# Performance work log

Hardware: AMD Instinct MI355X
Metric: run time of the kernel (lower is better)

Reference implementation:

```python
import jax, jax.numpy as jnp
import numpy as np

E, D, DFF = 8, 1024, 4096

def setup_inputs() -> dict:
    key = jax.random.key(0)
    ks = jax.random.split(key, 10)
    s = 0.02
    return {
        "x":  jax.random.normal(ks[0], (4, 2048, D), dtype=jnp.float32),
        "Wr": jax.random.normal(ks[1], (D, E), dtype=jnp.float32) * s,
        "br": jnp.zeros((E,), dtype=jnp.float32),
        "W1": jax.random.normal(ks[2], (E, D, DFF), dtype=jnp.float32) * s,
        "b1": jnp.zeros((E, DFF), dtype=jnp.float32),
        "W2": jax.random.normal(ks[3], (E, D, DFF), dtype=jnp.float32) * s,
        "b2": jnp.zeros((E, DFF), dtype=jnp.float32),
        "W3": jax.random.normal(ks[4], (E, DFF, D), dtype=jnp.float32) * s,
        "b3": jnp.zeros((E, D), dtype=jnp.float32),
    }

def reference(x, Wr, br, W1, b1, W2, b2, W3, b3):
    b, s, d = x.shape
    xt = x.reshape(b * s, d)                       # [T, D]
    logits = xt @ Wr + br                          # [T, E]
    pr, idx = jax.lax.top_k(logits, 2)             # [T, 2]
    w = jax.nn.softmax(pr, axis=-1)                # softmax over the 2 selected experts
    # combine weight per (token, expert): sum of routing weights where expert selected
    onehot = jax.nn.one_hot(idx, W1.shape[0], dtype=x.dtype)  # [T, 2, E]
    cw = jnp.einsum('tk,tke->te', w, onehot)       # [T, E]
    y = jnp.zeros_like(xt)
    for e in range(W1.shape[0]):                   # small fixed expert loop
        h = jax.nn.silu(xt @ W1[e] + b1[e]) * (xt @ W2[e] + b2[e])  # SwiGLU [T, DFF]
        y = y + (h @ W3[e] + b3[e]) * cw[:, e:e + 1]
    return y.reshape(b, s, d)
```

## Files before the change

kernel.cpp:

```cpp
#include <hip/hip_runtime.h>

#define T_TOK 8192
#define DIM   1024
#define DFF_  4096
#define NE    8
#define MAXT  144

typedef float  f32x4 __attribute__((ext_vector_type(4)));
typedef __bf16 b16x8 __attribute__((ext_vector_type(8)));
typedef unsigned short u16x4 __attribute__((ext_vector_type(4)));

__device__ __forceinline__ unsigned short f2bf(float f) {
  union { float f; unsigned int u; } v; v.f = f;
  unsigned int r = v.u + 0x7fffu + ((v.u >> 16) & 1u);
  return (unsigned short)(r >> 16);
}

__device__ __forceinline__ void gload_lds16(const void* g, void* l) {
  __builtin_amdgcn_global_load_lds((const __attribute__((address_space(1))) void*)g,
                                   (__attribute__((address_space(3))) void*)l,
                                   16, 0, 0);
}

#define DRAIN_VMCNT() asm volatile("s_waitcnt vmcnt(0)" ::: "memory")

__global__ __launch_bounds__(256) void transpose_cvt(const float* __restrict__ src,
                                                     unsigned short* __restrict__ dst,
                                                     int R, int C) {
  __shared__ float tile[64][68];
  size_t mat = (size_t)blockIdx.z * R * C;
  int c0 = blockIdx.x * 64, r0 = blockIdx.y * 64;
  int t = threadIdx.x;
  int rcol = (t & 15) * 4, rrow = t >> 4;
  const float* s = src + mat + (size_t)r0 * C + c0;
#pragma unroll
  for (int i = 0; i < 4; i++) {
    int r = rrow + i * 16;
    f32x4 v = *(const f32x4*)(s + (size_t)r * C + rcol);
    *(f32x4*)(&tile[r][rcol]) = v;
  }
  __syncthreads();
  unsigned short* d = dst + mat + (size_t)c0 * R + r0;
  int wrow4 = (t & 15) * 4, wcol = t >> 4;
#pragma unroll
  for (int i = 0; i < 4; i++) {
    int cc = wcol + i * 16;
    u16x4 o;
    o[0] = f2bf(tile[wrow4 + 0][cc]);
    o[1] = f2bf(tile[wrow4 + 1][cc]);
    o[2] = f2bf(tile[wrow4 + 2][cc]);
    o[3] = f2bf(tile[wrow4 + 3][cc]);
    *(u16x4*)(&d[(size_t)cc * R + wrow4]) = o;
  }
}

__global__ __launch_bounds__(256) void router_k(const float* __restrict__ x,
                                                const float* __restrict__ Wr,
                                                const float* __restrict__ br,
                                                unsigned short* __restrict__ Xbf,
                                                int* __restrict__ top2e,
                                                float* __restrict__ top2w,
                                                int* __restrict__ counts) {
  __shared__ int lcnt[NE];
  if (threadIdx.x < NE) lcnt[threadIdx.x] = 0;
  __syncthreads();
  int wid = threadIdx.x >> 6, lane = threadIdx.x & 63;
  int t = blockIdx.x * 4 + wid;
  const float* xr = x + (size_t)t * DIM;
  unsigned short* xb = Xbf + (size_t)t * DIM;
  float s[NE];
#pragma unroll
  for (int e = 0; e < NE; e++) s[e] = 0.f;
  for (int i = 0; i < DIM / 64; i++) {
    int dd = i * 64 + lane;
    float xv = xr[dd];
    xb[dd] = f2bf(xv);
    const float* w = Wr + (size_t)dd * NE;
#pragma unroll
    for (int e = 0; e < NE; e++) s[e] += xv * w[e];
  }
#pragma unroll
  for (int m = 32; m >= 1; m >>= 1) {
#pragma unroll
    for (int e = 0; e < NE; e++) s[e] += __shfl_xor(s[e], m, 64);
  }
  if (lane == 0) {
#pragma unroll
    for (int e = 0; e < NE; e++) s[e] += br[e];
    int e0 = 0;
#pragma unroll
    for (int e = 1; e < NE; e++) if (s[e] > s[e0]) e0 = e;
    int e1 = (e0 == 0) ? 1 : 0;
#pragma unroll
    for (int e = 0; e < NE; e++) if (e != e0 && s[e] > s[e1]) e1 = e;
    float w0 = 1.f / (1.f + expf(s[e1] - s[e0]));
    top2e[2 * t] = e0; top2e[2 * t + 1] = e1;
    top2w[2 * t] = w0; top2w[2 * t + 1] = 1.f - w0;
    atomicAdd(&lcnt[e0], 1);
    atomicAdd(&lcnt[e1], 1);
  }
  __syncthreads();
  if (threadIdx.x < NE) atomicAdd(&counts[threadIdx.x], lcnt[threadIdx.x]);
}

__global__ void scan_build(int* __restrict__ ctrl) {
  if (threadIdx.x != 0 || blockIdx.x != 0) return;
  int* counts = ctrl;
  int* offsets = ctrl + 8;
  int* cursors = ctrl + 16;
  int* nt256 = ctrl + 24;
  int* nt128 = ctrl + 25;
  int* tE256 = ctrl + 32;
  int* tM256 = ctrl + 32 + MAXT;
  int* tE128 = ctrl + 32 + 2 * MAXT;
  int* tM128 = ctrl + 32 + 3 * MAXT;
  int o = 0;
  for (int e = 0; e < NE; e++) { offsets[e] = o; cursors[e] = o; o += counts[e]; }
  int a = 0, b = 0;
  for (int e = 0; e < NE; e++) {
    for (int m0 = 0; m0 < counts[e]; m0 += 256) { tE256[a] = e; tM256[a] = m0; a++; }
    for (int m0 = 0; m0 < counts[e]; m0 += 128) { tE128[b] = e; tM128[b] = m0; b++; }
  }
  nt256[0] = a;
  nt128[0] = b;
}

__global__ __launch_bounds__(256) void scatter_k(const int* __restrict__ top2e,
                                                 const float* __restrict__ top2w,
                                                 int* __restrict__ cursors,
                                                 int* __restrict__ list_tok,
                                                 float* __restrict__ list_w) {
  __shared__ int lcnt[NE];
  __shared__ int lbase[NE];
  int tid = threadIdx.x;
  if (tid < NE) lcnt[tid] = 0;
  __syncthreads();
  int t = blockIdx.x * 256 + tid;
  int e0 = top2e[2 * t], e1 = top2e[2 * t + 1];
  int r0 = atomicAdd(&lcnt[e0], 1);
  int r1 = atomicAdd(&lcnt[e1], 1);
  __syncthreads();
  if (tid < NE) lbase[tid] = atomicAdd(&cursors[tid], lcnt[tid]);
  __syncthreads();
  int p0 = lbase[e0] + r0, p1 = lbase[e1] + r1;
  list_tok[p0] = t; list_w[p0] = top2w[2 * t];
  list_tok[p1] = t; list_w[p1] = top2w[2 * t + 1];
}

__global__ __launch_bounds__(1024, 4) void gemm1_k(const unsigned short* __restrict__ Xbf,
                                                   const unsigned short* __restrict__ W1T,
                                                   const unsigned short* __restrict__ W2T,
                                                   const float* __restrict__ b1,
                                                   const float* __restrict__ b2,
                                                   unsigned short* __restrict__ H,
                                                   const int* __restrict__ list_tok,
                                                   const int* __restrict__ ctrl) {
  const int* counts = ctrl; const int* offsets = ctrl + 8;
  const int* ntile = ctrl + 24;
  const int* tileE = ctrl + 32; const int* tileM = ctrl + 32 + MAXT;
  int bt = blockIdx.y;
  if (bt >= ntile[0]) return;
  int e = tileE[bt], m0 = tileM[bt];
  int Me = counts[e], off = offsets[e];
  int n0 = blockIdx.x * 128;

  __shared__ unsigned short lds[2][32768];

  int tid = threadIdx.x, lane = tid & 63, wid = tid >> 6;
  int wr = wid >> 2, wc = wid & 3;

  const unsigned short* gsrc[4];
  unsigned ldsoff[4];
  {
    int lr = lane >> 3;
    int sc = ((lane & 7) ^ (lane >> 3)) * 8;
#pragma unroll
    for (int j = 0; j < 4; j++) {
      int c = wid * 4 + j;
      ldsoff[j] = c * 512;
      if (c < 32) {
        int r = c * 8 + lr;
        int tok = (m0 + r < Me) ? list_tok[off + m0 + r] : list_tok[off];
        gsrc[j] = Xbf + (size_t)tok * DIM + sc;
      } else if (c < 48) {
        int n = n0 + (c - 32) * 8 + lr;
        gsrc[j] = W1T + ((size_t)e * DFF_ + n) * DIM + sc;
      } else {
        int n = n0 + (c - 48) * 8 + lr;
        gsrc[j] = W2T + ((size_t)e * DFF_ + n) * DIM + sc;
      }
    }
  }

  unsigned aoff[2][4], boff[2][2];
  {
    int colg = lane >> 4;
#pragma unroll
    for (int kk = 0; kk < 2; kk++) {
#pragma unroll
      for (int m = 0; m < 4; m++) {
        int row = wr * 64 + m * 16 + (lane & 15);
        aoff[kk][m] = row * 64 + (((kk * 4 + colg) ^ (row & 7)) * 8);
      }
#pragma unroll
      for (int n = 0; n < 2; n++) {
        int row = wc * 32 + n * 16 + (lane & 15);
        boff[kk][n] = 16384 + row * 64 + (((kk * 4 + colg) ^ (row & 7)) * 8);
      }
    }
  }

  f32x4 acc1[4][2], acc2[4][2];
#pragma unroll
  for (int i = 0; i < 4; i++)
#pragma unroll
    for (int j = 0; j < 2; j++) {
      acc1[i][j] = f32x4{0.f, 0.f, 0.f, 0.f};
      acc2[i][j] = f32x4{0.f, 0.f, 0.f, 0.f};
    }

  auto compute = [&](const unsigned short* base) {
#pragma unroll
    for (int kk = 0; kk < 2; kk++) {
      b16x8 aF[4], bF1[2], bF2[2];
#pragma unroll
      for (int m = 0; m < 4; m++) aF[m] = *(const b16x8*)(base + aoff[kk][m]);
#pragma unroll
      for (int n = 0; n < 2; n++) {
        bF1[n] = *(const b16x8*)(base + boff[kk][n]);
        bF2[n] = *(const b16x8*)(base + boff[kk][n] + 8192);
      }
#pragma unroll
      for (int m = 0; m < 4; m++)
#pragma unroll
        for (int n = 0; n < 2; n++) {
          acc1[m][n] = __builtin_amdgcn_mfma_f32_16x16x32_bf16(aF[m], bF1[n], acc1[m][n], 0, 0, 0);
          acc2[m][n] = __builtin_amdgcn_mfma_f32_16x16x32_bf16(aF[m], bF2[n], acc2[m][n], 0, 0, 0);
        }
    }
  };

#pragma unroll
  for (int j = 0; j < 4; j++) gload_lds16(gsrc[j], (void*)(&lds[0][ldsoff[j]]));
  DRAIN_VMCNT();
  __syncthreads();

  int cur = 0;
  const int NK = DIM / 64;
  for (int kt = 0; kt < NK; kt++) {
    if (kt + 1 < NK) {
#pragma unroll
      for (int j = 0; j < 4; j++)
        gload_lds16(gsrc[j] + (kt + 1) * 64, (void*)(&lds[cur ^ 1][ldsoff[j]]));
    }
    compute(&lds[cur][0]);
    DRAIN_VMCNT();
    __syncthreads();
    cur ^= 1;
  }

#pragma unroll
  for (int n = 0; n < 2; n++) {
    int col = n0 + wc * 32 + n * 16 + (lane & 15);
    float bb1 = b1[e * DFF_ + col], bb2 = b2[e * DFF_ + col];
#pragma unroll
    for (int m = 0; m < 4; m++) {
      int rbase = wr * 64 + m * 16 + (lane >> 4) * 4;
#pragma unroll
      for (int r = 0; r < 4; r++) {
        int rr = rbase + r;
        if (m0 + rr < Me) {
          float c1 = acc1[m][n][r] + bb1;
          float c2 = acc2[m][n][r] + bb2;
          float h = c1 * c2 / (1.f + __expf(-c1));
          H[(size_t)(off + m0 + rr) * DFF_ + col] = f2bf(h);
        }
      }
    }
  }
}

__global__ __launch_bounds__(512) void gemm2_k(const unsigned short* __restrict__ H,
                                               const unsigned short* __restrict__ W3T,
                                               const float* __restrict__ b3,
                                               const int* __restrict__ list_tok,
                                               const float* __restrict__ list_w,
                                               float* __restrict__ y,
                                               const int* __restrict__ ctrl) {
  const int* counts = ctrl; const int* offsets = ctrl + 8;
  const int* ntile = ctrl + 25;
  const int* tileE = ctrl + 32 + 2 * MAXT;
  const int* tileM = ctrl + 32 + 3 * MAXT;
  int bt = blockIdx.y;
  if (bt >= ntile[0]) return;
  int e = tileE[bt], m0 = tileM[bt];
  int Me = counts[e], off = offsets[e];
  int n0 = blockIdx.x * 128;

  __shared__ unsigned short lds[2][2 * 128 * 64];

  int tid = threadIdx.x, lane = tid & 63, wid = tid >> 6;
  int wr = wid >> 2, wc = wid & 3;

  const unsigned short* gsrc[4];
  unsigned ldsoff[4];
  {
    int lr = lane >> 3;
    int sc = ((lane & 7) ^ (lane >> 3)) * 8;
#pragma unroll
    for (int j = 0; j < 4; j++) {
      int c = wid * 4 + j;
      ldsoff[j] = c * 512;
      if (c < 16) {
        int r = c * 8 + lr;
        int pos = (m0 + r < Me) ? (off + m0 + r) : off;
        gsrc[j] = H + (size_t)pos * DFF_ + sc;
      } else {
        int n = n0 + (c - 16) * 8 + lr;
        gsrc[j] = W3T + ((size_t)e * DIM + n) * DFF_ + sc;
      }
    }
  }

  unsigned aoff[2][4], boff[2][2];
  {
    int colg = lane >> 4;
#pragma unroll
    for (int kk = 0; kk < 2; kk++) {
#pragma unroll
      for (int fi = 0; fi < 4; fi++) {
        int row = wr * 64 + fi * 16 + (lane & 15);
        aoff[kk][fi] = row * 64 + (((kk * 4 + colg) ^ (row & 7)) * 8);
      }
#pragma unroll
      for (int fj = 0; fj < 2; fj++) {
        int row = wc * 32 + fj * 16 + (lane & 15);
        boff[kk][fj] = 128 * 64 + row * 64 + (((kk * 4 + colg) ^ (row & 7)) * 8);
      }
    }
  }

  f32x4 acc[4][2];
#pragma unroll
  for (int i = 0; i < 4; i++)
#pragma unroll
    for (int j = 0; j < 2; j++) acc[i][j] = f32x4{0.f, 0.f, 0.f, 0.f};

  auto compute = [&](const unsigned short* base) {
#pragma unroll
    for (int kk = 0; kk < 2; kk++) {
      b16x8 aF[4], bF[2];
#pragma unroll
      for (int fi = 0; fi < 4; fi++) aF[fi] = *(const b16x8*)(base + aoff[kk][fi]);
#pragma unroll
      for (int fj = 0; fj < 2; fj++) bF[fj] = *(const b16x8*)(base + boff[kk][fj]);
#pragma unroll
      for (int fi = 0; fi < 4; fi++)
#pragma unroll
        for (int fj = 0; fj < 2; fj++)
          acc[fi][fj] = __builtin_amdgcn_mfma_f32_16x16x32_bf16(aF[fi], bF[fj], acc[fi][fj], 0, 0, 0);
    }
  };

#pragma unroll
  for (int j = 0; j < 4; j++) gload_lds16(gsrc[j], (void*)(&lds[0][ldsoff[j]]));
  DRAIN_VMCNT();
  __syncthreads();

  int cur = 0;
  const int NK = DFF_ / 64;
  for (int kt = 0; kt < NK; kt++) {
    if (kt + 1 < NK) {
#pragma unroll
      for (int j = 0; j < 4; j++)
        gload_lds16(gsrc[j] + (kt + 1) * 64, (void*)(&lds[cur ^ 1][ldsoff[j]]));
    }
    compute(&lds[cur][0]);
    DRAIN_VMCNT();
    __syncthreads();
    cur ^= 1;
  }

#pragma unroll
  for (int fi = 0; fi < 4; fi++)
#pragma unroll
    for (int fj = 0; fj < 2; fj++) {
      int col = n0 + wc * 32 + fj * 16 + (lane & 15);
      float bb3 = b3[e * DIM + col];
      int rbase = wr * 64 + fi * 16 + (lane >> 4) * 4;
#pragma unroll
      for (int r = 0; r < 4; r++) {
        int rr = rbase + r;
        if (m0 + rr < Me) {
          int pos = off + m0 + rr;
          float v = list_w[pos] * (acc[fi][fj][r] + bb3);
          atomicAdd(&y[(size_t)list_tok[pos] * DIM + col], v);
        }
      }
    }
}

extern "C" void kernel_launch(void* const* d_in, const int* in_sizes, int n_in,
                              void* d_out, int out_size, void* d_ws, size_t ws_size,
                              hipStream_t stream) {
  (void)in_sizes; (void)n_in; (void)ws_size;
  const float* x  = (const float*)d_in[0];
  const float* Wr = (const float*)d_in[1];
  const float* br = (const float*)d_in[2];
  const float* W1 = (const float*)d_in[3];
  const float* b1 = (const float*)d_in[4];
  const float* W2 = (const float*)d_in[5];
  const float* b2 = (const float*)d_in[6];
  const float* W3 = (const float*)d_in[7];
  const float* b3 = (const float*)d_in[8];
  float* y = (float*)d_out;
  char* ws = (char*)d_ws;

  const size_t matB = (size_t)NE * DFF_ * DIM * 2;
  size_t oW1T = 0;
  size_t oW2T = oW1T + matB;
  size_t oXbf = oW2T + matB;
  size_t oH   = oXbf + (size_t)T_TOK * DIM * 2;
  size_t oT2e = oH + (size_t)2 * T_TOK * DFF_ * 2;
  size_t oT2w = oT2e + (size_t)2 * T_TOK * 4;
  size_t oLtk = oT2w + (size_t)2 * T_TOK * 4;
  size_t oLw  = oLtk + (size_t)2 * T_TOK * 4;
  size_t oCtl = oLw + (size_t)2 * T_TOK * 4;

  unsigned short* W1T = (unsigned short*)(ws + oW1T);
  unsigned short* W2T = (unsigned short*)(ws + oW2T);
  unsigned short* W3T = (unsigned short*)(ws + oW1T);
  unsigned short* Xbf = (unsigned short*)(ws + oXbf);
  unsigned short* Hb  = (unsigned short*)(ws + oH);
  int*   top2e = (int*)(ws + oT2e);
  float* top2w = (float*)(ws + oT2w);
  int*   ltok  = (int*)(ws + oLtk);
  float* lw    = (float*)(ws + oLw);
  int*   ctrl  = (int*)(ws + oCtl);

  hipMemsetAsync(y, 0, (size_t)out_size * 4, stream);
  hipMemsetAsync(ctrl, 0, (32 + 4 * MAXT) * 4, stream);

  transpose_cvt<<<dim3(DFF_ / 64, DIM / 64, NE), 256, 0, stream>>>(W1, W1T, DIM, DFF_);
  transpose_cvt<<<dim3(DFF_ / 64, DIM / 64, NE), 256, 0, stream>>>(W2, W2T, DIM, DFF_);
  router_k<<<dim3(T_TOK / 4), 256, 0, stream>>>(x, Wr, br, Xbf, top2e, top2w, ctrl);
  scan_build<<<dim3(1), 64, 0, stream>>>(ctrl);
  scatter_k<<<dim3(T_TOK / 256), 256, 0, stream>>>(top2e, top2w, ctrl + 16, ltok, lw);
  gemm1_k<<<dim3(DFF_ / 128, 71), 1024, 0, stream>>>(Xbf, W1T, W2T, b1, b2, Hb, ltok, ctrl);
  transpose_cvt<<<dim3(DIM / 64, DFF_ / 64, NE), 256, 0, stream>>>(W3, W3T, DFF_, DIM);
  gemm2_k<<<dim3(DIM / 128, MAXT - 8), 512, 0, stream>>>(Hb, W3T, b3, ltok, lw, y, ctrl);
}
```

Before: 739.6 us.

## Enlarge gemm2 tiles to 256x256 with 1024 threads and shared 256-row tile list

The second expert GEMM moves from 128-row by 128-col tiles with 512 threads to 256-row by 256-col tiles with 1024 threads, reusing the 256-row tile list already built for gemm1. The 128-row tile list is dropped from the scan kernel and the control memset shrinks to match. Each wave now computes a 64x64 output block with 16 MFMA accumulators, which raises arithmetic intensity per LDS load and cuts the number of times H and W3T are reread. The cost is 128 KB of LDS per block and fewer blocks in flight, which lowers occupancy and increases padding waste for partially filled expert tiles.

```diff
diff --git a/kernel.cpp b/kernel.cpp
--- a/kernel.cpp
+++ b/kernel.cpp
@@ -109,20 +109,14 @@
   int* offsets = ctrl + 8;
   int* cursors = ctrl + 16;
   int* nt256 = ctrl + 24;
-  int* nt128 = ctrl + 25;
   int* tE256 = ctrl + 32;
   int* tM256 = ctrl + 32 + MAXT;
-  int* tE128 = ctrl + 32 + 2 * MAXT;
-  int* tM128 = ctrl + 32 + 3 * MAXT;
   int o = 0;
   for (int e = 0; e < NE; e++) { offsets[e] = o; cursors[e] = o; o += counts[e]; }
-  int a = 0, b = 0;
-  for (int e = 0; e < NE; e++) {
+  int a = 0;
+  for (int e = 0; e < NE; e++)
     for (int m0 = 0; m0 < counts[e]; m0 += 256) { tE256[a] = e; tM256[a] = m0; a++; }
-    for (int m0 = 0; m0 < counts[e]; m0 += 128) { tE128[b] = e; tM128[b] = m0; b++; }
-  }
   nt256[0] = a;
-  nt128[0] = b;
 }
 
 __global__ __launch_bounds__(256) void scatter_k(const int* __restrict__ top2e,
@@ -280,24 +274,23 @@
   }
 }
 
-__global__ __launch_bounds__(512) void gemm2_k(const unsigned short* __restrict__ H,
-                                               const unsigned short* __restrict__ W3T,
-                                               const float* __restrict__ b3,
-                                               const int* __restrict__ list_tok,
-                                               const float* __restrict__ list_w,
-                                               float* __restrict__ y,
-                                               const int* __restrict__ ctrl) {
+__global__ __launch_bounds__(1024, 4) void gemm2_k(const unsigned short* __restrict__ H,
+                                                   const unsigned short* __restrict__ W3T,
+                                                   const float* __restrict__ b3,
+                                                   const int* __restrict__ list_tok,
+                                                   const float* __restrict__ list_w,
+                                                   float* __restrict__ y,
+                                                   const int* __restrict__ ctrl) {
   const int* counts = ctrl; const int* offsets = ctrl + 8;
-  const int* ntile = ctrl + 25;
-  const int* tileE = ctrl + 32 + 2 * MAXT;
-  const int* tileM = ctrl + 32 + 3 * MAXT;
+  const int* ntile = ctrl + 24;
+  const int* tileE = ctrl + 32; const int* tileM = ctrl + 32 + MAXT;
   int bt = blockIdx.y;
   if (bt >= ntile[0]) return;
   int e = tileE[bt], m0 = tileM[bt];
   int Me = counts[e], off = offsets[e];
-  int n0 = blockIdx.x * 128;
-
-  __shared__ unsigned short lds[2][2 * 128 * 64];
+  int n0 = blockIdx.x * 256;
+
+  __shared__ unsigned short lds[2][32768];
 
   int tid = threadIdx.x, lane = tid & 63, wid = tid >> 6;
   int wr = wid >> 2, wc = wid & 3;
@@ -311,54 +304,54 @@
     for (int j = 0; j < 4; j++) {
       int c = wid * 4 + j;
       ldsoff[j] = c * 512;
-      if (c < 16) {
+      if (c < 32) {
         int r = c * 8 + lr;
         int pos = (m0 + r < Me) ? (off + m0 + r) : off;
         gsrc[j] = H + (size_t)pos * DFF_ + sc;
       } else {
-        int n = n0 + (c - 16) * 8 + lr;
+        int n = n0 + (c - 32) * 8 + lr;
         gsrc[j] = W3T + ((size_t)e * DIM + n) * DFF_ + sc;
       }
     }
   }
 
-  unsigned aoff[2][4], boff[2][2];
+  unsigned aoff[2][4], boff[2][4];
   {
     int colg = lane >> 4;
 #pragma unroll
     for (int kk = 0; kk < 2; kk++) {
 #pragma unroll
-      for (int fi = 0; fi < 4; fi++) {
-        int row = wr * 64 + fi * 16 + (lane & 15);
-        aoff[kk][fi] = row * 64 + (((kk * 4 + colg) ^ (row & 7)) * 8);
-      }
-#pragma unroll
-      for (int fj = 0; fj < 2; fj++) {
-        int row = wc * 32 + fj * 16 + (lane & 15);
-        boff[kk][fj] = 128 * 64 + row * 64 + (((kk * 4 + colg) ^ (row & 7)) * 8);
-      }
-    }
-  }
-
-  f32x4 acc[4][2];
+      for (int m = 0; m < 4; m++) {
+        int row = wr * 64 + m * 16 + (lane & 15);
+        aoff[kk][m] = row * 64 + (((kk * 4 + colg) ^ (row & 7)) * 8);
+      }
+#pragma unroll
+      for (int n = 0; n < 4; n++) {
+        int row = wc * 64 + n * 16 + (lane & 15);
+        boff[kk][n] = 16384 + row * 64 + (((kk * 4 + colg) ^ (row & 7)) * 8);
+      }
+    }
+  }
+
+  f32x4 acc[4][4];
 #pragma unroll
   for (int i = 0; i < 4; i++)
 #pragma unroll
-    for (int j = 0; j < 2; j++) acc[i][j] = f32x4{0.f, 0.f, 0.f, 0.f};
+    for (int j = 0; j < 4; j++) acc[i][j] = f32x4{0.f, 0.f, 0.f, 0.f};
 
   auto compute = [&](const unsigned short* base) {
 #pragma unroll
     for (int kk = 0; kk < 2; kk++) {
-      b16x8 aF[4], bF[2];
-#pragma unroll
-      for (int fi = 0; fi < 4; fi++) aF[fi] = *(const b16x8*)(base + aoff[kk][fi]);
-#pragma unroll
-      for (int fj = 0; fj < 2; fj++) bF[fj] = *(const b16x8*)(base + boff[kk][fj]);
-#pragma unroll
-      for (int fi = 0; fi < 4; fi++)
-#pragma unroll
-        for (int fj = 0; fj < 2; fj++)
-          acc[fi][fj] = __builtin_amdgcn_mfma_f32_16x16x32_bf16(aF[fi], bF[fj], acc[fi][fj], 0, 0, 0);
+      b16x8 aF[4], bF[4];
+#pragma unroll
+      for (int m = 0; m < 4; m++) aF[m] = *(const b16x8*)(base + aoff[kk][m]);
+#pragma unroll
+      for (int n = 0; n < 4; n++) bF[n] = *(const b16x8*)(base + boff[kk][n]);
+#pragma unroll
+      for (int m = 0; m < 4; m++)
+#pragma unroll
+        for (int n = 0; n < 4; n++)
+          acc[m][n] = __builtin_amdgcn_mfma_f32_16x16x32_bf16(aF[m], bF[n], acc[m][n], 0, 0, 0);
     }
   };
 
@@ -382,22 +375,23 @@
   }
 
 #pragma unroll
-  for (int fi = 0; fi < 4; fi++)
-#pragma unroll
-    for (int fj = 0; fj < 2; fj++) {
-      int col = n0 + wc * 32 + fj * 16 + (lane & 15);
-      float bb3 = b3[e * DIM + col];
-      int rbase = wr * 64 + fi * 16 + (lane >> 4) * 4;
+  for (int n = 0; n < 4; n++) {
+    int col = n0 + wc * 64 + n * 16 + (lane & 15);
+    float bb3 = b3[e * DIM + col];
+#pragma unroll
+    for (int m = 0; m < 4; m++) {
+      int rbase = wr * 64 + m * 16 + (lane >> 4) * 4;
 #pragma unroll
       for (int r = 0; r < 4; r++) {
         int rr = rbase + r;
         if (m0 + rr < Me) {
           int pos = off + m0 + rr;
-          float v = list_w[pos] * (acc[fi][fj][r] + bb3);
+          float v = list_w[pos] * (acc[m][n][r] + bb3);
           atomicAdd(&y[(size_t)list_tok[pos] * DIM + col], v);
         }
       }
     }
+  }
 }
 
 extern "C" void kernel_launch(void* const* d_in, const int* in_sizes, int n_in,
@@ -439,7 +433,7 @@
   int*   ctrl  = (int*)(ws + oCtl);
 
   hipMemsetAsync(y, 0, (size_t)out_size * 4, stream);
-  hipMemsetAsync(ctrl, 0, (32 + 4 * MAXT) * 4, stream);
+  hipMemsetAsync(ctrl, 0, (32 + 2 * MAXT) * 4, stream);
 
   transpose_cvt<<<dim3(DFF_ / 64, DIM / 64, NE), 256, 0, stream>>>(W1, W1T, DIM, DFF_);
   transpose_cvt<<<dim3(DFF_ / 64, DIM / 64, NE), 256, 0, stream>>>(W2, W2T, DIM, DFF_);
@@ -448,5 +442,5 @@
   scatter_k<<<dim3(T_TOK / 256), 256, 0, stream>>>(top2e, top2w, ctrl + 16, ltok, lw);
   gemm1_k<<<dim3(DFF_ / 128, 71), 1024, 0, stream>>>(Xbf, W1T, W2T, b1, b2, Hb, ltok, ctrl);
   transpose_cvt<<<dim3(DIM / 64, DFF_ / 64, NE), 256, 0, stream>>>(W3, W3T, DFF_, DIM);
-  gemm2_k<<<dim3(DIM / 128, MAXT - 8), 512, 0, stream>>>(Hb, W3T, b3, ltok, lw, y, ctrl);
-}
+  gemm2_k<<<dim3(DIM / 256, 71), 1024, 0, stream>>>(Hb, W3T, b3, ltok, lw, y, ctrl);
+}
```

Result: faster. 706.7 us (-4.4%).
